# Performance work log

Hardware: AMD Instinct MI355X
Metric: run time of the kernel (lower is better)

## Reference

```python
import jax, jax.numpy as jnp
import numpy as np

N = 50000      # nodes
E = 800000     # edges (avg degree 16)
F_IN = 128     # input feature dim
HID = 128      # 2 * out_classes
OUT = 64       # out_classes


def setup_inputs() -> dict:
    key = jax.random.key(0)
    ks = jax.random.split(key, 12)
    x = jax.random.normal(ks[0], (N, F_IN), jnp.float32)
    edge_index = jax.random.randint(ks[1], (2, E), 0, N, jnp.int32)
    def lin(k, fi, fo):
        return jax.random.normal(k, (fi, fo), jnp.float32) / np.float32(np.sqrt(fi))
    return {
        "x": x,
        "edge_index": edge_index,
        "W1": lin(ks[2], F_IN, HID), "b1": jnp.zeros((HID,), jnp.float32),
        "W2": lin(ks[3], HID, HID),  "b2": jnp.zeros((HID,), jnp.float32),
        "W3": lin(ks[4], HID, HID),  "b3": jnp.zeros((HID,), jnp.float32),
        "jk_w": jax.random.normal(ks[5], (3,), jnp.float32),
        "fc_W": lin(ks[6], HID, OUT), "fc_b": jnp.zeros((OUT,), jnp.float32),
    }


def _gcn_conv(h, W, b, row, col, n):
    """PyG GCNConv: linear -> add self-loops -> sym-normalized aggregate -> bias."""
    h = h @ W                                        # [n, d_out]
    loops = jnp.arange(n, dtype=row.dtype)
    r = jnp.concatenate([row, loops])                # sources
    c = jnp.concatenate([col, loops])                # targets
    deg = jax.ops.segment_sum(jnp.ones_like(c, h.dtype), c, num_segments=n)
    dinv = jnp.where(deg > 0, jax.lax.rsqrt(deg), 0.0)
    norm = dinv[r] * dinv[c]                         # [E+n]
    msg = h[r] * norm[:, None]                       # gather + scale
    return jax.ops.segment_sum(msg, c, num_segments=n) + b


def _neighbor_mean(h, row, col, n):
    """sample_neighbors with scale_factor=2: exact mean over out-neighbors,
    own feature when degree == 0 (top-k branch is provably dead code)."""
    s = jax.ops.segment_sum(h[col], row, num_segments=n)
    deg = jax.ops.segment_sum(jnp.ones_like(row, h.dtype), row, num_segments=n)
    mean = s / jnp.maximum(deg, 1.0)[:, None]
    return jnp.where((deg > 0)[:, None], mean, h)


def reference(x, edge_index, W1, b1, W2, b2, W3, b3, jk_w, fc_W, fc_b):
    row, col = edge_index[0], edge_index[1]
    n = x.shape[0]
    # layer 0: GCN -> ReLU -> (dropout: eval identity) -> neighbor sampling
    h0 = jax.nn.relu(_gcn_conv(x, W1, b1, row, col, n))
    h0 = _neighbor_mean(h0, row, col, n)
    # layer 1: GCN -> ReLU; historical-activation update is identity on first call
    h1 = jax.nn.relu(_gcn_conv(h0, W2, b2, row, col, n))
    # layer 2
    h2 = jax.nn.relu(_gcn_conv(h1, W3, b3, row, col, n))
    # dynamic JK aggregation
    w = jax.nn.softmax(jk_w)
    h = w[0] * h0 + w[1] * h1 + w[2] * h2
    return h @ fc_W + fc_b
```

## Files before the change

### kernel.cpp

```cpp
#include <hip/hip_runtime.h>
#include <stdint.h>

typedef unsigned int  uint32;
typedef unsigned short u16;

typedef short bfx8 __attribute__((ext_vector_type(8)));
typedef float f32x4 __attribute__((ext_vector_type(4)));
typedef uint32 u32x4 __attribute__((ext_vector_type(4)));

#define NBP 256
#define CH  2048
#define BS  4608

__device__ __forceinline__ float b2f(u16 u) {
    union { uint32 i; float f; } v; v.i = ((uint32)u) << 16; return v.f;
}
__device__ __forceinline__ u16 f2b(float f) {
    union { float f; uint32 i; } v; v.f = f;
    uint32 u = v.i;
    return (u16)((u + 0x7fffu + ((u >> 16) & 1u)) >> 16);
}
__device__ __forceinline__ float blo(uint32 u) {
    union { uint32 i; float f; } v; v.i = u << 16; return v.f;
}
__device__ __forceinline__ float bhi(uint32 u) {
    union { uint32 i; float f; } v; v.i = u & 0xffff0000u; return v.f;
}
__device__ __forceinline__ uint32 packbf(float a, float b) {
    return (uint32)f2b(a) | ((uint32)f2b(b) << 16);
}
__device__ __forceinline__ void splitf(float x, u16& h, u16& l) {
    h = f2b(x);
    l = f2b(x - b2f(h));
}
__device__ __forceinline__ void acc4(float* s, u32x4 v) {
    s[0] += blo(v.x); s[1] += bhi(v.x);
    s[2] += blo(v.y); s[3] += bhi(v.y);
    s[4] += blo(v.z); s[5] += bhi(v.z);
    s[6] += blo(v.w); s[7] += bhi(v.w);
}
__device__ __forceinline__ void acc4f(float* s, u32x4 v, float d) {
    s[0] = fmaf(blo(v.x), d, s[0]); s[1] = fmaf(bhi(v.x), d, s[1]);
    s[2] = fmaf(blo(v.y), d, s[2]); s[3] = fmaf(bhi(v.y), d, s[3]);
    s[4] = fmaf(blo(v.z), d, s[4]); s[5] = fmaf(bhi(v.z), d, s[5]);
    s[6] = fmaf(blo(v.w), d, s[6]); s[7] = fmaf(bhi(v.w), d, s[7]);
}

__global__ __launch_bounds__(256) void k_init(
    int* __restrict__ curC, int* __restrict__ curR,
    const float* __restrict__ W1, const float* __restrict__ W2,
    const float* __restrict__ W3, const float* __restrict__ fcW,
    u16* __restrict__ WTh, u16* __restrict__ WTl, int WTN) {
    int t = threadIdx.x;
    if (blockIdx.x == 0) {
        curC[t] = t * BS;
        curR[t] = t * BS;
        return;
    }
    int i = ((int)blockIdx.x - 1) * 256 + t;
    if (i >= WTN) return;
    float w;
    if (i < 3 * 16384) {
        int m = i >> 14, j = i & 16383;
        int fo = j >> 7, fi = j & 127;
        const float* W = (m == 0) ? W1 : (m == 1) ? W2 : W3;
        w = W[fi * 128 + fo];
    } else {
        int j = i - 3 * 16384;
        int fo = j >> 7, fi = j & 127;
        w = fcW[fi * 64 + fo];
    }
    u16 h, l; splitf(w, h, l);
    WTh[i] = h; WTl[i] = l;
}

__global__ __launch_bounds__(256) void k_partC(
    const int* __restrict__ row, const int* __restrict__ col, int E,
    int* __restrict__ curC, int* __restrict__ curR,
    uint32* __restrict__ partC, uint32* __restrict__ partR) {
    __shared__ uint32 stagedC[CH], stagedR[CH];
    __shared__ int hp[NBP], expk[NBP], curp[NBP], runC[NBP], runR[NBP];
    __shared__ int wsum[4];
    int t = threadIdx.x;
    int lane = t & 63, wid = t >> 6;
    int base = blockIdx.x * CH;
    int n = E - base; if (n > CH) n = CH;

    int er[8], ec[8];
#pragma unroll
    for (int j = 0; j < 8; ++j) {
        int i = t + j * 256;
        if (i < n) { er[j] = row[base + i]; ec[j] = col[base + i]; }
        else er[j] = -1;
    }
    hp[t] = 0;
    __syncthreads();
#pragma unroll
    for (int j = 0; j < 8; ++j) {
        if (er[j] >= 0) {
            atomicAdd(&hp[ec[j] >> 8], 1);
            atomicAdd(&hp[er[j] >> 8], 0x10000);
        }
    }
    __syncthreads();
    int v = hp[t];
    int x = v;
#pragma unroll
    for (int d = 1; d < 64; d <<= 1) {
        int u = __shfl_up(x, d);
        if (lane >= d) x += u;
    }
    if (lane == 63) wsum[wid] = x;
    __syncthreads();
    int add = 0;
    for (int i = 0; i < wid; ++i) add += wsum[i];
    int ex = x + add - v;
    expk[t] = ex;
    curp[t] = ex;
    int vC = v & 0xffff, vR = v >> 16;
    runC[t] = vC ? atomicAdd(&curC[t], vC) : 0;
    runR[t] = vR ? atomicAdd(&curR[t], vR) : 0;
    __syncthreads();
#pragma unroll
    for (int j = 0; j < 8; ++j) {
        if (er[j] >= 0) {
            int cb = ec[j] >> 8, rb = er[j] >> 8;
            int pC = atomicAdd(&curp[cb], 1) & 0xffff;
            stagedC[pC] = ((uint32)ec[j] << 16) | (uint32)er[j];
            int pR = atomicAdd(&curp[rb], 0x10000) >> 16;
            stagedR[pR] = ((uint32)er[j] << 16) | (uint32)ec[j];
        }
    }
    __syncthreads();
    for (int i = t; i < n; i += 256) {
        uint32 pv = stagedC[i];
        int b = pv >> 24;
        partC[runC[b] + (i - (expk[b] & 0xffff))] = pv;
    }
    for (int i = t; i < n; i += 256) {
        uint32 pv = stagedR[i];
        int b = pv >> 24;
        partR[runR[b] + (i - (expk[b] >> 16))] = pv;
    }
}

__global__ __launch_bounds__(256) void k_fillDg0(
    const uint32* __restrict__ partC, const uint32* __restrict__ partR,
    const int* __restrict__ curC, const int* __restrict__ curR,
    int* __restrict__ off_in, int* __restrict__ end_in,
    int* __restrict__ off_out, int* __restrict__ end_out,
    u16* __restrict__ csr_src, u16* __restrict__ csr_dst,
    float* __restrict__ dinv, int NB, int N,
    const float* __restrict__ A, const u16* __restrict__ WTh,
    const u16* __restrict__ WTl, u16* __restrict__ G) {
    __shared__ int cnt[NBP], cur[NBP];
    __shared__ int wsum[4];
    int t = threadIdx.x;

    if ((int)blockIdx.x < 2 * NB) {
        int part = ((int)blockIdx.x >= NB) ? 1 : 0;
        int b = (int)blockIdx.x - part * NB;
        const uint32* arr = part ? partR : partC;
        const int* curA   = part ? curR : curC;
        int* offA         = part ? off_out : off_in;
        int* endA         = part ? end_out : end_in;
        u16* csr          = part ? csr_dst : csr_src;
        int lane = t & 63, wid = t >> 6;
        int base = b * BS, end = curA[b];
        cnt[t] = 0;
        __syncthreads();
        for (int i = base + t; i < end; i += 256)
            atomicAdd(&cnt[(arr[i] >> 16) & 255], 1);
        __syncthreads();
        int v = cnt[t];
        int x = v;
#pragma unroll
        for (int d = 1; d < 64; d <<= 1) {
            int u = __shfl_up(x, d);
            if (lane >= d) x += u;
        }
        if (lane == 63) wsum[wid] = x;
        __syncthreads();
        int add = 0;
        for (int i = 0; i < wid; ++i) add += wsum[i];
        int ex = x + add - v;
        cur[t] = ex;
        int node = (b << 8) + t;
        if (node < N) {
            offA[node] = base + ex;
            endA[node] = base + ex + v;
            if (part == 0) dinv[node] = rsqrtf((float)(v + 1));
        }
        __syncthreads();
        for (int i = base + t; i < end; i += 256) {
            uint32 pv = arr[i];
            int local = (pv >> 16) & 255;
            int pos = atomicAdd(&cur[local], 1);
            csr[base + pos] = (u16)(pv & 0xffffu);
        }
        return;
    }

    {
        int gb = (int)blockIdx.x - 2 * NB;
        const int lane = t & 63;
        const int q = lane >> 4, l = lane & 15;
        int rbase = gb * 128 + (t >> 6) * 32;
        if (rbase >= N) return;
        int r0 = rbase + l;      if (r0 >= N) r0 = N - 1;
        int r1 = rbase + 16 + l; if (r1 >= N) r1 = N - 1;

        f32x4 acc[2][8];
#pragma unroll
        for (int i = 0; i < 2; ++i)
#pragma unroll
            for (int j = 0; j < 8; ++j) acc[i][j] = (f32x4){0.f, 0.f, 0.f, 0.f};

#pragma unroll
        for (int kc = 0; kc < 4; ++kc) {
            int k0 = kc * 32 + q * 8;
            bfx8 ah0, ah1;
            {
                f32x4 a = *(const f32x4*)(A + (size_t)r0 * 128 + k0);
                f32x4 b = *(const f32x4*)(A + (size_t)r0 * 128 + k0 + 4);
                float xx[8] = {a[0], a[1], a[2], a[3], b[0], b[1], b[2], b[3]};
#pragma unroll
                for (int j = 0; j < 8; ++j) ah0[j] = (short)f2b(xx[j]);
            }
            {
                f32x4 a = *(const f32x4*)(A + (size_t)r1 * 128 + k0);
                f32x4 b = *(const f32x4*)(A + (size_t)r1 * 128 + k0 + 4);
                float xx[8] = {a[0], a[1], a[2], a[3], b[0], b[1], b[2], b[3]};
#pragma unroll
                for (int j = 0; j < 8; ++j) ah1[j] = (short)f2b(xx[j]);
            }
#pragma unroll
            for (int ct = 0; ct < 8; ++ct) {
                bfx8 bh = *(const bfx8*)(WTh + (ct * 16 + l) * 128 + k0);
                bfx8 bl = *(const bfx8*)(WTl + (ct * 16 + l) * 128 + k0);
                acc[0][ct] = __builtin_amdgcn_mfma_f32_16x16x32_bf16(ah0, bh, acc[0][ct], 0, 0, 0);
                acc[0][ct] = __builtin_amdgcn_mfma_f32_16x16x32_bf16(ah0, bl, acc[0][ct], 0, 0, 0);
                acc[1][ct] = __builtin_amdgcn_mfma_f32_16x16x32_bf16(ah1, bh, acc[1][ct], 0, 0, 0);
                acc[1][ct] = __builtin_amdgcn_mfma_f32_16x16x32_bf16(ah1, bl, acc[1][ct], 0, 0, 0);
            }
        }
#pragma unroll
        for (int rs = 0; rs < 2; ++rs) {
#pragma unroll
            for (int rr = 0; rr < 4; ++rr) {
                int rw = rbase + rs * 16 + q * 4 + rr;
                if (rw < N) {
#pragma unroll
                    for (int ct = 0; ct < 8; ++ct)
                        G[(size_t)rw * 128 + ct * 16 + l] = f2b(acc[rs][ct][rr]);
                }
            }
        }
    }
}

__global__ __launch_bounds__(256) void k_gemm1p(
    const u16* __restrict__ Ah,
    const u16* __restrict__ WTh, const u16* __restrict__ WTl,
    const float* __restrict__ dinv, u16* __restrict__ G, int M) {
    const int lane = threadIdx.x & 63;
    const int q = lane >> 4, l = lane & 15;
    int rbase = blockIdx.x * 128 + (threadIdx.x >> 6) * 32;
    if (rbase >= M) return;
    int r0 = rbase + l;      if (r0 >= M) r0 = M - 1;
    int r1 = rbase + 16 + l; if (r1 >= M) r1 = M - 1;

    f32x4 acc[2][8];
#pragma unroll
    for (int i = 0; i < 2; ++i)
#pragma unroll
        for (int j = 0; j < 8; ++j) acc[i][j] = (f32x4){0.f, 0.f, 0.f, 0.f};

#pragma unroll
    for (int kc = 0; kc < 4; ++kc) {
        int k0 = kc * 32 + q * 8;
        bfx8 ah0 = *(const bfx8*)(Ah + (size_t)r0 * 128 + k0);
        bfx8 ah1 = *(const bfx8*)(Ah + (size_t)r1 * 128 + k0);
#pragma unroll
        for (int ct = 0; ct < 8; ++ct) {
            bfx8 bh = *(const bfx8*)(WTh + (ct * 16 + l) * 128 + k0);
            bfx8 bl = *(const bfx8*)(WTl + (ct * 16 + l) * 128 + k0);
            acc[0][ct] = __builtin_amdgcn_mfma_f32_16x16x32_bf16(ah0, bh, acc[0][ct], 0, 0, 0);
            acc[0][ct] = __builtin_amdgcn_mfma_f32_16x16x32_bf16(ah0, bl, acc[0][ct], 0, 0, 0);
            acc[1][ct] = __builtin_amdgcn_mfma_f32_16x16x32_bf16(ah1, bh, acc[1][ct], 0, 0, 0);
            acc[1][ct] = __builtin_amdgcn_mfma_f32_16x16x32_bf16(ah1, bl, acc[1][ct], 0, 0, 0);
        }
    }
#pragma unroll
    for (int rs = 0; rs < 2; ++rs) {
#pragma unroll
        for (int rr = 0; rr < 4; ++rr) {
            int rw = rbase + rs * 16 + q * 4 + rr;
            if (rw < M) {
                float dv = dinv[rw];
#pragma unroll
                for (int ct = 0; ct < 8; ++ct)
                    G[(size_t)rw * 128 + ct * 16 + l] = f2b(acc[rs][ct][rr] * dv);
            }
        }
    }
}

__global__ __launch_bounds__(256) void k_agg0(
    const u32x4* __restrict__ g4, const u16* __restrict__ csr,
    const int* __restrict__ off, const int* __restrict__ endo,
    const float* __restrict__ dinv,
    const float* __restrict__ bias, u32x4* __restrict__ outH4, int n) {
    int w = (blockIdx.x * 256 + threadIdx.x) >> 6;
    if (w >= n) return;
    int lane = threadIdx.x & 63;
    int gq = lane >> 4, c = lane & 15;
    float s[8];
#pragma unroll
    for (int k = 0; k < 8; ++k) s[k] = 0.f;
    int e = off[w], e1 = endo[w];
    for (; e + 16 <= e1; e += 16) {
        int ix[4];
#pragma unroll
        for (int j = 0; j < 4; ++j) ix[j] = csr[e + j * 4 + gq];
        u32x4 vv[4];
        float dd[4];
#pragma unroll
        for (int j = 0; j < 4; ++j) { vv[j] = g4[(size_t)ix[j] * 16 + c]; dd[j] = dinv[ix[j]]; }
#pragma unroll
        for (int j = 0; j < 4; ++j) acc4f(s, vv[j], dd[j]);
    }
    for (; e < e1; e += 4) {
        int idx = e + gq;
        if (idx < e1) {
            int ii = csr[idx];
            acc4f(s, g4[(size_t)ii * 16 + c], dinv[ii]);
        }
    }
#pragma unroll
    for (int k = 0; k < 8; ++k) {
        s[k] += __shfl_xor(s[k], 16);
        s[k] += __shfl_xor(s[k], 32);
    }
    if (lane < 16) {
        float dc = dinv[w];
        u32x4 sv = g4[(size_t)w * 16 + lane];
        acc4f(s, sv, dc);
        const f32x4* B4 = (const f32x4*)bias;
        f32x4 ba = B4[lane * 2], bb = B4[lane * 2 + 1];
        float o[8];
#pragma unroll
        for (int k = 0; k < 4; ++k) o[k] = fmaxf(fmaf(s[k], dc, ba[k]), 0.f);
#pragma unroll
        for (int k = 0; k < 4; ++k) o[4 + k] = fmaxf(fmaf(s[4 + k], dc, bb[k]), 0.f);
        u32x4 ov;
        ov.x = packbf(o[0], o[1]); ov.y = packbf(o[2], o[3]);
        ov.z = packbf(o[4], o[5]); ov.w = packbf(o[6], o[7]);
        outH4[(size_t)w * 16 + lane] = ov;
    }
}

__global__ __launch_bounds__(256) void k_agg(
    const u32x4* __restrict__ g4, const u16* __restrict__ csr,
    const int* __restrict__ off, const int* __restrict__ endo,
    const float* __restrict__ dinv,
    const float* __restrict__ bias, u32x4* __restrict__ outH4, int n) {
    int w = (blockIdx.x * 256 + threadIdx.x) >> 6;
    if (w >= n) return;
    int lane = threadIdx.x & 63;
    int gq = lane >> 4, c = lane & 15;
    float s[8];
#pragma unroll
    for (int k = 0; k < 8; ++k) s[k] = 0.f;
    int e = off[w], e1 = endo[w];
    for (; e + 16 <= e1; e += 16) {
        int ix[4];
#pragma unroll
        for (int j = 0; j < 4; ++j) ix[j] = csr[e + j * 4 + gq];
        u32x4 vv[4];
#pragma unroll
        for (int j = 0; j < 4; ++j) vv[j] = g4[(size_t)ix[j] * 16 + c];
#pragma unroll
        for (int j = 0; j < 4; ++j) acc4(s, vv[j]);
    }
    for (; e < e1; e += 4) {
        int idx = e + gq;
        if (idx < e1) {
            int ii = csr[idx];
            acc4(s, g4[(size_t)ii * 16 + c]);
        }
    }
#pragma unroll
    for (int k = 0; k < 8; ++k) {
        s[k] += __shfl_xor(s[k], 16);
        s[k] += __shfl_xor(s[k], 32);
    }
    if (lane < 16) {
        u32x4 sv = g4[(size_t)w * 16 + lane];
        acc4(s, sv);
        float dc = dinv[w];
        const f32x4* B4 = (const f32x4*)bias;
        f32x4 ba = B4[lane * 2], bb = B4[lane * 2 + 1];
        float o[8];
#pragma unroll
        for (int k = 0; k < 4; ++k) o[k] = fmaxf(fmaf(s[k], dc, ba[k]), 0.f);
#pragma unroll
        for (int k = 0; k < 4; ++k) o[4 + k] = fmaxf(fmaf(s[4 + k], dc, bb[k]), 0.f);
        u32x4 ov;
        ov.x = packbf(o[0], o[1]); ov.y = packbf(o[2], o[3]);
        ov.z = packbf(o[4], o[5]); ov.w = packbf(o[6], o[7]);
        outH4[(size_t)w * 16 + lane] = ov;
    }
}

__global__ __launch_bounds__(256) void k_mean(
    const u32x4* __restrict__ h4, const u16* __restrict__ csr,
    const int* __restrict__ off, const int* __restrict__ endo,
    u32x4* __restrict__ outH4, int n) {
    int w = (blockIdx.x * 256 + threadIdx.x) >> 6;
    if (w >= n) return;
    int lane = threadIdx.x & 63;
    int gq = lane >> 4, c = lane & 15;
    float s[8];
#pragma unroll
    for (int k = 0; k < 8; ++k) s[k] = 0.f;
    int e = off[w], e1 = endo[w];
    int d = e1 - e;
    for (; e + 16 <= e1; e += 16) {
        int ix[4];
#pragma unroll
        for (int j = 0; j < 4; ++j) ix[j] = csr[e + j * 4 + gq];
        u32x4 vv[4];
#pragma unroll
        for (int j = 0; j < 4; ++j) vv[j] = h4[(size_t)ix[j] * 16 + c];
#pragma unroll
        for (int j = 0; j < 4; ++j) acc4(s, vv[j]);
    }
    for (; e < e1; e += 4) {
        int idx = e + gq;
        if (idx < e1) {
            int ii = csr[idx];
            acc4(s, h4[(size_t)ii * 16 + c]);
        }
    }
#pragma unroll
    for (int k = 0; k < 8; ++k) {
        s[k] += __shfl_xor(s[k], 16);
        s[k] += __shfl_xor(s[k], 32);
    }
    if (lane < 16) {
        u32x4 ov;
        if (d > 0) {
            float inv = 1.f / (float)d;
            ov.x = packbf(s[0] * inv, s[1] * inv);
            ov.y = packbf(s[2] * inv, s[3] * inv);
            ov.z = packbf(s[4] * inv, s[5] * inv);
            ov.w = packbf(s[6] * inv, s[7] * inv);
        } else {
            ov = h4[(size_t)w * 16 + lane];
        }
        outH4[(size_t)w * 16 + lane] = ov;
    }
}

__global__ __launch_bounds__(256) void k_final(
    const u16* __restrict__ h0, const u16* __restrict__ h1,
    const u16* __restrict__ h2, const float* __restrict__ jkw,
    const u16* __restrict__ fcWTh, const u16* __restrict__ fcWTl,
    const float* __restrict__ fcb, float* __restrict__ out, int M) {
    float a0 = jkw[0], a1 = jkw[1], a2 = jkw[2];
    float mx = fmaxf(a0, fmaxf(a1, a2));
    float e0 = expf(a0 - mx), e1 = expf(a1 - mx), e2 = expf(a2 - mx);
    float inv = 1.f / (e0 + e1 + e2);
    float w0 = e0 * inv, w1 = e1 * inv, w2 = e2 * inv;

    const int lane = threadIdx.x & 63;
    const int q = lane >> 4, l = lane & 15;
    int rbase = blockIdx.x * 128 + (threadIdx.x >> 6) * 32;
    if (rbase >= M) return;
    int r0 = rbase + l;      if (r0 >= M) r0 = M - 1;
    int r1 = rbase + 16 + l; if (r1 >= M) r1 = M - 1;

    f32x4 acc[2][4];
#pragma unroll
    for (int i = 0; i < 2; ++i)
#pragma unroll
        for (int j = 0; j < 4; ++j) acc[i][j] = (f32x4){0.f, 0.f, 0.f, 0.f};

    union U8 { bfx8 v; u16 u[8]; };

#pragma unroll
    for (int kc = 0; kc < 4; ++kc) {
        int k0 = kc * 32 + q * 8;
        bfx8 ah[2];
        const int rr2[2] = {r0, r1};
#pragma unroll
        for (int half = 0; half < 2; ++half) {
            size_t o = (size_t)rr2[half] * 128 + k0;
            U8 x0, x1, x2, rh;
            x0.v = *(const bfx8*)(h0 + o);
            x1.v = *(const bfx8*)(h1 + o);
            x2.v = *(const bfx8*)(h2 + o);
#pragma unroll
            for (int j = 0; j < 8; ++j) {
                float c = w0 * b2f(x0.u[j]) + w1 * b2f(x1.u[j]) + w2 * b2f(x2.u[j]);
                rh.u[j] = f2b(c);
            }
            ah[half] = rh.v;
        }
#pragma unroll
        for (int ct = 0; ct < 4; ++ct) {
            bfx8 bh = *(const bfx8*)(fcWTh + (ct * 16 + l) * 128 + k0);
            bfx8 bl = *(const bfx8*)(fcWTl + (ct * 16 + l) * 128 + k0);
#pragma unroll
            for (int half = 0; half < 2; ++half) {
                acc[half][ct] = __builtin_amdgcn_mfma_f32_16x16x32_bf16(ah[half], bh, acc[half][ct], 0, 0, 0);
                acc[half][ct] = __builtin_amdgcn_mfma_f32_16x16x32_bf16(ah[half], bl, acc[half][ct], 0, 0, 0);
            }
        }
    }
#pragma unroll
    for (int rs = 0; rs < 2; ++rs) {
#pragma unroll
        for (int rr = 0; rr < 4; ++rr) {
            int rw = rbase + rs * 16 + q * 4 + rr;
            if (rw < M) {
#pragma unroll
                for (int ct = 0; ct < 4; ++ct) {
                    int cc = ct * 16 + l;
                    out[(size_t)rw * 64 + cc] = acc[rs][ct][rr] + fcb[cc];
                }
            }
        }
    }
}

extern "C" void kernel_launch(void* const* d_in, const int* in_sizes, int n_in,
                              void* d_out, int out_size, void* d_ws, size_t ws_size,
                              hipStream_t stream) {
    const int N = in_sizes[0] / 128;
    const int E = in_sizes[1] / 2;
    const int NB = (N + 255) >> 8;

    const float* x    = (const float*)d_in[0];
    const int* row    = (const int*)d_in[1];
    const int* col    = row + E;
    const float* W1   = (const float*)d_in[2];
    const float* b1   = (const float*)d_in[3];
    const float* W2   = (const float*)d_in[4];
    const float* b2   = (const float*)d_in[5];
    const float* W3   = (const float*)d_in[6];
    const float* b3   = (const float*)d_in[7];
    const float* jkw  = (const float*)d_in[8];
    const float* fcW  = (const float*)d_in[9];
    const float* fcb  = (const float*)d_in[10];
    float* outp       = (float*)d_out;

    char* ws = (char*)d_ws;
    size_t off = 0;
    auto alloc = [&](size_t bytes) -> char* {
        char* p = ws + off;
        off += (bytes + 255) & ~(size_t)255;
        return p;
    };
    int* curC   = (int*)alloc((size_t)NBP * sizeof(int));
    int* curR   = (int*)alloc((size_t)NBP * sizeof(int));
    int* off_in  = (int*)alloc((size_t)N * sizeof(int));
    int* end_in  = (int*)alloc((size_t)N * sizeof(int));
    int* off_out = (int*)alloc((size_t)N * sizeof(int));
    int* end_out = (int*)alloc((size_t)N * sizeof(int));
    uint32* partC = (uint32*)alloc((size_t)NBP * BS * sizeof(uint32));
    uint32* partR = (uint32*)alloc((size_t)NBP * BS * sizeof(uint32));
    u16* csr_src = (u16*)alloc((size_t)NBP * BS * sizeof(u16));
    u16* csr_dst = (u16*)alloc((size_t)NBP * BS * sizeof(u16));
    float* dinv  = (float*)alloc((size_t)N * sizeof(float));
    const int WTN = 3 * 16384 + 8192;
    u16* WTh = (u16*)alloc((size_t)WTN * sizeof(u16));
    u16* WTl = (u16*)alloc((size_t)WTN * sizeof(u16));
    size_t FB = (size_t)N * 128 * sizeof(u16);
    u16* gbuf = (u16*)alloc(FB);
    u16* t0   = (u16*)alloc(FB);
    u16* h0   = (u16*)alloc(FB);
    u16* h1   = (u16*)alloc(FB);
    u16* h2   = (u16*)alloc(FB);

    const int B = 256;
    int Gh = (E + CH - 1) / CH;
    int Gg = (N + 127) / 128;
    int Gwt = (WTN + B - 1) / B;

    k_init<<<1 + Gwt, B, 0, stream>>>(curC, curR, W1, W2, W3, fcW, WTh, WTl, WTN);
    k_partC<<<Gh, B, 0, stream>>>(row, col, E, curC, curR, partC, partR);
    k_fillDg0<<<2 * NB + Gg, B, 0, stream>>>(partC, partR, curC, curR,
                                             off_in, end_in, off_out, end_out,
                                             csr_src, csr_dst, dinv, NB, N,
                                             x, WTh, WTl, gbuf);

    int aggG = (N + 3) / 4;

    k_agg0<<<aggG, B, 0, stream>>>((const u32x4*)gbuf, csr_src, off_in, end_in, dinv,
                                   b1, (u32x4*)t0, N);
    k_mean<<<aggG, B, 0, stream>>>((const u32x4*)t0, csr_dst, off_out, end_out,
                                   (u32x4*)h0, N);
    k_gemm1p<<<Gg, B, 0, stream>>>(h0, WTh + 16384, WTl + 16384, dinv, gbuf, N);
    k_agg<<<aggG, B, 0, stream>>>((const u32x4*)gbuf, csr_src, off_in, end_in, dinv,
                                  b2, (u32x4*)h1, N);
    k_gemm1p<<<Gg, B, 0, stream>>>(h1, WTh + 2 * 16384, WTl + 2 * 16384, dinv, gbuf, N);
    k_agg<<<aggG, B, 0, stream>>>((const u32x4*)gbuf, csr_src, off_in, end_in, dinv,
                                  b3, (u32x4*)h2, N);
    k_final<<<Gg, B, 0, stream>>>(h0, h1, h2, jkw,
                                  WTh + 3 * 16384, WTl + 3 * 16384, fcb, outp, N);
}
```

Baseline: 327.3 us.

## Split feature matrices into two 64-column halves to shrink gather working set

Feature buffers are stored as two contiguous [N,64] bf16 halves instead of interleaved [N,128] rows, and every aggregation kernel launches twice as many blocks, each processing one half. The GEMM and final kernels are updated to read and write this split layout. The goal is to halve the random-gather footprint per kernel pass, so each half (about 6.4MB) fits better in L2/MALL, in exchange for each gather fetching 8 bytes per lane instead of 16 and CSR indices being read twice.

```diff
diff --git a/kernel.cpp b/kernel.cpp
--- a/kernel.cpp
+++ b/kernel.cpp
@@ -6,11 +6,12 @@
 
 typedef short bfx8 __attribute__((ext_vector_type(8)));
 typedef float f32x4 __attribute__((ext_vector_type(4)));
-typedef uint32 u32x4 __attribute__((ext_vector_type(4)));
+typedef uint32 u32x2 __attribute__((ext_vector_type(2)));
 
 #define NBP 256
 #define CH  2048
 #define BS  4608
+
 
 __device__ __forceinline__ float b2f(u16 u) {
     union { uint32 i; float f; } v; v.i = ((uint32)u) << 16; return v.f;
@@ -33,17 +34,13 @@
     h = f2b(x);
     l = f2b(x - b2f(h));
 }
-__device__ __forceinline__ void acc4(float* s, u32x4 v) {
+__device__ __forceinline__ void acc2(float* s, u32x2 v) {
     s[0] += blo(v.x); s[1] += bhi(v.x);
     s[2] += blo(v.y); s[3] += bhi(v.y);
-    s[4] += blo(v.z); s[5] += bhi(v.z);
-    s[6] += blo(v.w); s[7] += bhi(v.w);
-}
-__device__ __forceinline__ void acc4f(float* s, u32x4 v, float d) {
+}
+__device__ __forceinline__ void acc2f(float* s, u32x2 v, float d) {
     s[0] = fmaf(blo(v.x), d, s[0]); s[1] = fmaf(bhi(v.x), d, s[1]);
     s[2] = fmaf(blo(v.y), d, s[2]); s[3] = fmaf(bhi(v.y), d, s[3]);
-    s[4] = fmaf(blo(v.z), d, s[4]); s[5] = fmaf(bhi(v.z), d, s[5]);
-    s[6] = fmaf(blo(v.w), d, s[6]); s[7] = fmaf(bhi(v.w), d, s[7]);
 }
 
 __global__ __launch_bounds__(256) void k_init(
@@ -205,6 +202,7 @@
         int gb = (int)blockIdx.x - 2 * NB;
         const int lane = t & 63;
         const int q = lane >> 4, l = lane & 15;
+        const size_t N64 = (size_t)N * 64;
         int rbase = gb * 128 + (t >> 6) * 32;
         if (rbase >= N) return;
         int r0 = rbase + l;      if (r0 >= N) r0 = N - 1;
@@ -252,7 +250,8 @@
                 if (rw < N) {
 #pragma unroll
                     for (int ct = 0; ct < 8; ++ct)
-                        G[(size_t)rw * 128 + ct * 16 + l] = f2b(acc[rs][ct][rr]);
+                        G[(size_t)(ct >> 2) * N64 + (size_t)rw * 64 + (ct & 3) * 16 + l]
+                            = f2b(acc[rs][ct][rr]);
                 }
             }
         }
@@ -265,6 +264,7 @@
     const float* __restrict__ dinv, u16* __restrict__ G, int M) {
     const int lane = threadIdx.x & 63;
     const int q = lane >> 4, l = lane & 15;
+    const size_t N64 = (size_t)M * 64;
     int rbase = blockIdx.x * 128 + (threadIdx.x >> 6) * 32;
     if (rbase >= M) return;
     int r0 = rbase + l;      if (r0 >= M) r0 = M - 1;
@@ -279,8 +279,9 @@
 #pragma unroll
     for (int kc = 0; kc < 4; ++kc) {
         int k0 = kc * 32 + q * 8;
-        bfx8 ah0 = *(const bfx8*)(Ah + (size_t)r0 * 128 + k0);
-        bfx8 ah1 = *(const bfx8*)(Ah + (size_t)r1 * 128 + k0);
+        size_t ao = (size_t)(kc >> 1) * N64 + (kc & 1) * 32 + q * 8;
+        bfx8 ah0 = *(const bfx8*)(Ah + ao + (size_t)r0 * 64);
+        bfx8 ah1 = *(const bfx8*)(Ah + ao + (size_t)r1 * 64);
 #pragma unroll
         for (int ct = 0; ct < 8; ++ct) {
             bfx8 bh = *(const bfx8*)(WTh + (ct * 16 + l) * 128 + k0);
@@ -300,166 +301,166 @@
                 float dv = dinv[rw];
 #pragma unroll
                 for (int ct = 0; ct < 8; ++ct)
-                    G[(size_t)rw * 128 + ct * 16 + l] = f2b(acc[rs][ct][rr] * dv);
+                    G[(size_t)(ct >> 2) * N64 + (size_t)rw * 64 + (ct & 3) * 16 + l]
+                        = f2b(acc[rs][ct][rr] * dv);
             }
         }
     }
 }
 
 __global__ __launch_bounds__(256) void k_agg0(
-    const u32x4* __restrict__ g4, const u16* __restrict__ csr,
+    const uint32* __restrict__ T, const u16* __restrict__ csr,
     const int* __restrict__ off, const int* __restrict__ endo,
     const float* __restrict__ dinv,
-    const float* __restrict__ bias, u32x4* __restrict__ outH4, int n) {
-    int w = (blockIdx.x * 256 + threadIdx.x) >> 6;
+    const float* __restrict__ bias, uint32* __restrict__ outT, int n, int G1) {
+    int blk = (int)blockIdx.x;
+    int p = (blk >= G1) ? 1 : 0;
+    int nb = blk - p * G1;
+    int w = nb * 4 + (int)(threadIdx.x >> 6);
     if (w >= n) return;
     int lane = threadIdx.x & 63;
     int gq = lane >> 4, c = lane & 15;
-    float s[8];
-#pragma unroll
-    for (int k = 0; k < 8; ++k) s[k] = 0.f;
+    const uint32* Tp = T + (size_t)p * n * 32;
+    float s[4] = {0.f, 0.f, 0.f, 0.f};
     int e = off[w], e1 = endo[w];
     for (; e + 16 <= e1; e += 16) {
         int ix[4];
 #pragma unroll
         for (int j = 0; j < 4; ++j) ix[j] = csr[e + j * 4 + gq];
-        u32x4 vv[4];
+        u32x2 vv[4];
         float dd[4];
 #pragma unroll
-        for (int j = 0; j < 4; ++j) { vv[j] = g4[(size_t)ix[j] * 16 + c]; dd[j] = dinv[ix[j]]; }
-#pragma unroll
-        for (int j = 0; j < 4; ++j) acc4f(s, vv[j], dd[j]);
+        for (int j = 0; j < 4; ++j) {
+            vv[j] = *(const u32x2*)(Tp + (size_t)ix[j] * 32 + c * 2);
+            dd[j] = dinv[ix[j]];
+        }
+#pragma unroll
+        for (int j = 0; j < 4; ++j) acc2f(s, vv[j], dd[j]);
     }
     for (; e < e1; e += 4) {
         int idx = e + gq;
         if (idx < e1) {
             int ii = csr[idx];
-            acc4f(s, g4[(size_t)ii * 16 + c], dinv[ii]);
-        }
-    }
-#pragma unroll
-    for (int k = 0; k < 8; ++k) {
+            acc2f(s, *(const u32x2*)(Tp + (size_t)ii * 32 + c * 2), dinv[ii]);
+        }
+    }
+#pragma unroll
+    for (int k = 0; k < 4; ++k) {
         s[k] += __shfl_xor(s[k], 16);
         s[k] += __shfl_xor(s[k], 32);
     }
     if (lane < 16) {
         float dc = dinv[w];
-        u32x4 sv = g4[(size_t)w * 16 + lane];
-        acc4f(s, sv, dc);
-        const f32x4* B4 = (const f32x4*)bias;
-        f32x4 ba = B4[lane * 2], bb = B4[lane * 2 + 1];
-        float o[8];
-#pragma unroll
-        for (int k = 0; k < 4; ++k) o[k] = fmaxf(fmaf(s[k], dc, ba[k]), 0.f);
-#pragma unroll
-        for (int k = 0; k < 4; ++k) o[4 + k] = fmaxf(fmaf(s[4 + k], dc, bb[k]), 0.f);
-        u32x4 ov;
+        u32x2 sv = *(const u32x2*)(Tp + (size_t)w * 32 + lane * 2);
+        acc2f(s, sv, dc);
+        f32x4 bb = *(const f32x4*)(bias + p * 64 + lane * 4);
+        float o[4];
+#pragma unroll
+        for (int k = 0; k < 4; ++k) o[k] = fmaxf(fmaf(s[k], dc, bb[k]), 0.f);
+        u32x2 ov;
         ov.x = packbf(o[0], o[1]); ov.y = packbf(o[2], o[3]);
-        ov.z = packbf(o[4], o[5]); ov.w = packbf(o[6], o[7]);
-        outH4[(size_t)w * 16 + lane] = ov;
+        *(u32x2*)(outT + (size_t)p * n * 32 + (size_t)w * 32 + lane * 2) = ov;
     }
 }
 
 __global__ __launch_bounds__(256) void k_agg(
-    const u32x4* __restrict__ g4, const u16* __restrict__ csr,
+    const uint32* __restrict__ T, const u16* __restrict__ csr,
     const int* __restrict__ off, const int* __restrict__ endo,
     const float* __restrict__ dinv,
-    const float* __restrict__ bias, u32x4* __restrict__ outH4, int n) {
-    int w = (blockIdx.x * 256 + threadIdx.x) >> 6;
+    const float* __restrict__ bias, uint32* __restrict__ outT, int n, int G1) {
+    int blk = (int)blockIdx.x;
+    int p = (blk >= G1) ? 1 : 0;
+    int nb = blk - p * G1;
+    int w = nb * 4 + (int)(threadIdx.x >> 6);
     if (w >= n) return;
     int lane = threadIdx.x & 63;
     int gq = lane >> 4, c = lane & 15;
-    float s[8];
-#pragma unroll
-    for (int k = 0; k < 8; ++k) s[k] = 0.f;
+    const uint32* Tp = T + (size_t)p * n * 32;
+    float s[4] = {0.f, 0.f, 0.f, 0.f};
     int e = off[w], e1 = endo[w];
     for (; e + 16 <= e1; e += 16) {
         int ix[4];
 #pragma unroll
         for (int j = 0; j < 4; ++j) ix[j] = csr[e + j * 4 + gq];
-        u32x4 vv[4];
-#pragma unroll
-        for (int j = 0; j < 4; ++j) vv[j] = g4[(size_t)ix[j] * 16 + c];
-#pragma unroll
-        for (int j = 0; j < 4; ++j) acc4(s, vv[j]);
+        u32x2 vv[4];
+#pragma unroll
+        for (int j = 0; j < 4; ++j) vv[j] = *(const u32x2*)(Tp + (size_t)ix[j] * 32 + c * 2);
+#pragma unroll
+        for (int j = 0; j < 4; ++j) acc2(s, vv[j]);
     }
     for (; e < e1; e += 4) {
         int idx = e + gq;
         if (idx < e1) {
             int ii = csr[idx];
-            acc4(s, g4[(size_t)ii * 16 + c]);
-        }
-    }
-#pragma unroll
-    for (int k = 0; k < 8; ++k) {
+            acc2(s, *(const u32x2*)(Tp + (size_t)ii * 32 + c * 2));
+        }
+    }
+#pragma unroll
+    for (int k = 0; k < 4; ++k) {
         s[k] += __shfl_xor(s[k], 16);
         s[k] += __shfl_xor(s[k], 32);
     }
     if (lane < 16) {
-        u32x4 sv = g4[(size_t)w * 16 + lane];
-        acc4(s, sv);
+        u32x2 sv = *(const u32x2*)(Tp + (size_t)w * 32 + lane * 2);
+        acc2(s, sv);
         float dc = dinv[w];
-        const f32x4* B4 = (const f32x4*)bias;
-        f32x4 ba = B4[lane * 2], bb = B4[lane * 2 + 1];
-        float o[8];
-#pragma unroll
-        for (int k = 0; k < 4; ++k) o[k] = fmaxf(fmaf(s[k], dc, ba[k]), 0.f);
-#pragma unroll
-        for (int k = 0; k < 4; ++k) o[4 + k] = fmaxf(fmaf(s[4 + k], dc, bb[k]), 0.f);
-        u32x4 ov;
+        f32x4 bb = *(const f32x4*)(bias + p * 64 + lane * 4);
+        float o[4];
+#pragma unroll
+        for (int k = 0; k < 4; ++k) o[k] = fmaxf(fmaf(s[k], dc, bb[k]), 0.f);
+        u32x2 ov;
         ov.x = packbf(o[0], o[1]); ov.y = packbf(o[2], o[3]);
-        ov.z = packbf(o[4], o[5]); ov.w = packbf(o[6], o[7]);
-        outH4[(size_t)w * 16 + lane] = ov;
+        *(u32x2*)(outT + (size_t)p * n * 32 + (size_t)w * 32 + lane * 2) = ov;
     }
 }
 
 __global__ __launch_bounds__(256) void k_mean(
-    const u32x4* __restrict__ h4, const u16* __restrict__ csr,
+    const uint32* __restrict__ T, const u16* __restrict__ csr,
     const int* __restrict__ off, const int* __restrict__ endo,
-    u32x4* __restrict__ outH4, int n) {
-    int w = (blockIdx.x * 256 + threadIdx.x) >> 6;
+    uint32* __restrict__ outT, int n, int G1) {
+    int blk = (int)blockIdx.x;
+    int p = (blk >= G1) ? 1 : 0;
+    int nb = blk - p * G1;
+    int w = nb * 4 + (int)(threadIdx.x >> 6);
     if (w >= n) return;
     int lane = threadIdx.x & 63;
     int gq = lane >> 4, c = lane & 15;
-    float s[8];
-#pragma unroll
-    for (int k = 0; k < 8; ++k) s[k] = 0.f;
+    const uint32* Tp = T + (size_t)p * n * 32;
+    float s[4] = {0.f, 0.f, 0.f, 0.f};
     int e = off[w], e1 = endo[w];
     int d = e1 - e;
     for (; e + 16 <= e1; e += 16) {
         int ix[4];
 #pragma unroll
         for (int j = 0; j < 4; ++j) ix[j] = csr[e + j * 4 + gq];
-        u32x4 vv[4];
-#pragma unroll
-        for (int j = 0; j < 4; ++j) vv[j] = h4[(size_t)ix[j] * 16 + c];
-#pragma unroll
-        for (int j = 0; j < 4; ++j) acc4(s, vv[j]);
+        u32x2 vv[4];
+#pragma unroll
+        for (int j = 0; j < 4; ++j) vv[j] = *(const u32x2*)(Tp + (size_t)ix[j] * 32 + c * 2);
+#pragma unroll
+        for (int j = 0; j < 4; ++j) acc2(s, vv[j]);
     }
     for (; e < e1; e += 4) {
         int idx = e + gq;
         if (idx < e1) {
             int ii = csr[idx];
-            acc4(s, h4[(size_t)ii * 16 + c]);
-        }
-    }
-#pragma unroll
-    for (int k = 0; k < 8; ++k) {
+            acc2(s, *(const u32x2*)(Tp + (size_t)ii * 32 + c * 2));
+        }
+    }
+#pragma unroll
+    for (int k = 0; k < 4; ++k) {
         s[k] += __shfl_xor(s[k], 16);
         s[k] += __shfl_xor(s[k], 32);
     }
     if (lane < 16) {
-        u32x4 ov;
+        u32x2 ov;
         if (d > 0) {
             float inv = 1.f / (float)d;
             ov.x = packbf(s[0] * inv, s[1] * inv);
             ov.y = packbf(s[2] * inv, s[3] * inv);
-            ov.z = packbf(s[4] * inv, s[5] * inv);
-            ov.w = packbf(s[6] * inv, s[7] * inv);
         } else {
-            ov = h4[(size_t)w * 16 + lane];
-        }
-        outH4[(size_t)w * 16 + lane] = ov;
+            ov = *(const u32x2*)(Tp + (size_t)w * 32 + lane * 2);
+        }
+        *(u32x2*)(outT + (size_t)p * n * 32 + (size_t)w * 32 + lane * 2) = ov;
     }
 }
 
@@ -476,6 +477,7 @@
 
     const int lane = threadIdx.x & 63;
     const int q = lane >> 4, l = lane & 15;
+    const size_t N64 = (size_t)M * 64;
     int rbase = blockIdx.x * 128 + (threadIdx.x >> 6) * 32;
     if (rbase >= M) return;
     int r0 = rbase + l;      if (r0 >= M) r0 = M - 1;
@@ -492,11 +494,12 @@
 #pragma unroll
     for (int kc = 0; kc < 4; ++kc) {
         int k0 = kc * 32 + q * 8;
+        size_t ao = (size_t)(kc >> 1) * N64 + (kc & 1) * 32 + q * 8;
         bfx8 ah[2];
         const int rr2[2] = {r0, r1};
 #pragma unroll
         for (int half = 0; half < 2; ++half) {
-            size_t o = (size_t)rr2[half] * 128 + k0;
+            size_t o = ao + (size_t)rr2[half] * 64;
             U8 x0, x1, x2, rh;
             x0.v = *(const bfx8*)(h0 + o);
             x1.v = *(const bfx8*)(h1 + o);
@@ -596,18 +599,19 @@
                                              csr_src, csr_dst, dinv, NB, N,
                                              x, WTh, WTl, gbuf);
 
-    int aggG = (N + 3) / 4;
-
-    k_agg0<<<aggG, B, 0, stream>>>((const u32x4*)gbuf, csr_src, off_in, end_in, dinv,
-                                   b1, (u32x4*)t0, N);
-    k_mean<<<aggG, B, 0, stream>>>((const u32x4*)t0, csr_dst, off_out, end_out,
-                                   (u32x4*)h0, N);
+    int G1 = (N + 3) / 4;
+    int aggG = 2 * G1;
+
+    k_agg0<<<aggG, B, 0, stream>>>((const uint32*)gbuf, csr_src, off_in, end_in, dinv,
+                                   b1, (uint32*)t0, N, G1);
+    k_mean<<<aggG, B, 0, stream>>>((const uint32*)t0, csr_dst, off_out, end_out,
+                                   (uint32*)h0, N, G1);
     k_gemm1p<<<Gg, B, 0, stream>>>(h0, WTh + 16384, WTl + 16384, dinv, gbuf, N);
-    k_agg<<<aggG, B, 0, stream>>>((const u32x4*)gbuf, csr_src, off_in, end_in, dinv,
-                                  b2, (u32x4*)h1, N);
+    k_agg<<<aggG, B, 0, stream>>>((const uint32*)gbuf, csr_src, off_in, end_in, dinv,
+                                  b2, (uint32*)h1, N, G1);
     k_gemm1p<<<Gg, B, 0, stream>>>(h1, WTh + 2 * 16384, WTl + 2 * 16384, dinv, gbuf, N);
-    k_agg<<<aggG, B, 0, stream>>>((const u32x4*)gbuf, csr_src, off_in, end_in, dinv,
-                                  b3, (u32x4*)h2, N);
+    k_agg<<<aggG, B, 0, stream>>>((const uint32*)gbuf, csr_src, off_in, end_in, dinv,
+                                  b3, (uint32*)h2, N, G1);
     k_final<<<Gg, B, 0, stream>>>(h0, h1, h2, jkw,
                                   WTh + 3 * 16384, WTl + 3 * 16384, fcb, outp, N);
 }
```

Result: slower. 389.5 us (+19.0%).
